# Kernel tuning notes

Measured on AMD Instinct MI355X. Metric: run time of the kernel, lower is better.

Reference implementation:

```python
import jax, jax.numpy as jnp
import numpy as np

K_MASK = -2.3819763e+38
B, T, D = 1, 2048, 3584
N, KH, H = 28, 4, 128  # query heads, kv heads, head_dim
ROPE_THETA = 1000000.0


def _rope_tables(t, h, theta):
    pos = jnp.arange(t, dtype=jnp.float32)[:, None]
    freq = theta ** (-jnp.arange(0, h, 2, dtype=jnp.float32) / h)[None, :]
    ang = pos * freq  # (T, H/2)
    return jnp.sin(ang)[None], jnp.cos(ang)[None]  # (1, T, H/2)


def apply_rotary_embedding(x, sin, cos):
    # x: (B,T,heads,H); sin/cos: (B,T,H/2)
    x1, x2 = x[..., : x.shape[-1] // 2], x[..., x.shape[-1] // 2 :]
    s, c = sin[:, :, None, :], cos[:, :, None, :]
    return jnp.concatenate([x1 * c - x2 * s, x2 * c + x1 * s], axis=-1)


def setup_inputs() -> dict:
    key = jax.random.key(0)
    ks = jax.random.split(key, 8)
    x = jax.random.normal(ks[0], (B, T, D), jnp.float32)
    attn_mask = jnp.tril(jnp.ones((T, T), jnp.bool_))[None]  # causal (B,T,S)
    sin, cos = _rope_tables(T, H, ROPE_THETA)
    std = 0.02
    wq = jax.random.normal(ks[1], (D, N, H), jnp.float32) * std
    wk = jax.random.normal(ks[2], (D, KH, H), jnp.float32) * std
    wv = jax.random.normal(ks[3], (D, KH, H), jnp.float32) * std
    wo = jax.random.normal(ks[4], (N, H, D), jnp.float32) * std
    q_bias = jax.random.normal(ks[5], (N * H,), jnp.float32) * std
    k_bias = jax.random.normal(ks[6], (KH * H,), jnp.float32) * std
    v_bias = jax.random.normal(ks[7], (KH * H,), jnp.float32) * std
    return {"x": x, "attn_mask": attn_mask, "sin": sin, "cos": cos,
            "wq": wq, "wk": wk, "wv": wv, "wo": wo,
            "q_bias": q_bias, "k_bias": k_bias, "v_bias": v_bias}


def reference(x, attn_mask, sin, cos, wq, wk, wv, wo, q_bias, k_bias, v_bias):
    b, t, _ = x.shape
    q = jnp.einsum('BTD,DNH->BTNH', x, wq) + q_bias.reshape(1, 1, N, H)
    k = jnp.einsum('BSD,DKH->BSKH', x, wk) + k_bias.reshape(1, 1, KH, H)
    v = jnp.einsum('BSD,DKH->BSKH', x, wv) + v_bias.reshape(1, 1, KH, H)
    q = apply_rotary_embedding(q, sin, cos)
    k = apply_rotary_embedding(k, sin, cos)
    g = N // KH  # GQA group size
    scale = H ** -0.5
    qg = q.reshape(b, t, KH, g, H)
    attn = jnp.einsum('BTHGD,BSHD->BHGTS', qg, k) * scale  # no KV repetition
    attn = attn.reshape(b, N, t, t)
    attn = jnp.where(attn_mask[:, None, :, :], attn, K_MASK)
    attn = jax.nn.softmax(attn.astype(jnp.float32), axis=-1).astype(k.dtype)
    attn = attn.reshape(b, KH, g, t, t)
    qkv = jnp.einsum('BHGTS,BSHD->BTHGD', attn, v).reshape(b, t, N, H)
    return jnp.einsum('BTNH,NHD->BTD', qkv, wo)
```

## Files before the change

kernel.cpp:

```cpp
#include <hip/hip_runtime.h>
#include <hip/hip_bf16.h>
#include <math.h>

#define Tn 2048
#define Dn 3584
#define NH 28
#define KHn 4
#define Hn 128
#define Gn 7
#define SCALE 0.08838834764831845f
#define LDC 4608
#define KOFF 3584
#define VOFF 4096
#define FBQ 128
#define FBS 64
#define NSPLIT 2
#define EXP_SHIFT 12.0f

typedef unsigned short u16;
typedef __attribute__((ext_vector_type(8))) short short8;
typedef __attribute__((ext_vector_type(4))) float floatx4;

__device__ __forceinline__ float bf_lo(unsigned int u) {
    union { unsigned int i; float f; } x; x.i = u << 16; return x.f;
}
__device__ __forceinline__ u16 f2bf(float f) {
    __hip_bfloat16 h = __float2bfloat16(f);
    return *reinterpret_cast<u16*>(&h);
}

__global__ void cast_f32_bf16(const float* __restrict__ in, u16* __restrict__ out, int n4)
{
    const int idx = blockIdx.x * blockDim.x + threadIdx.x;
    if (idx >= n4) return;
    const float4 f = ((const float4*)in)[idx];
    ((ushort4*)out)[idx] = make_ushort4(f2bf(f.x), f2bf(f.y), f2bf(f.z), f2bf(f.w));
}

__global__ __launch_bounds__(256) void transpose_cast(
    const float* __restrict__ in, u16* __restrict__ out, int R, int C, int ldo)
{
    __shared__ float ts[32][33];
    const int tid = threadIdx.x;
    const int c0 = blockIdx.x * 32, r0 = blockIdx.y * 32;
    const int tx = tid & 31, ty = tid >> 5;
    #pragma unroll
    for (int i = 0; i < 4; ++i)
        ts[ty + i * 8][tx] = in[(size_t)(r0 + ty + i * 8) * C + c0 + tx];
    __syncthreads();
    #pragma unroll
    for (int i = 0; i < 4; ++i)
        out[(size_t)(c0 + ty + i * 8) * ldo + r0 + tx] = f2bf(ts[tx][ty + i * 8]);
}

__global__ __launch_bounds__(256) void transpose_v(
    const u16* __restrict__ qkv, u16* __restrict__ vt)
{
    __shared__ u16 ts[32][33];
    const int tid = threadIdx.x;
    const int s0 = blockIdx.x * 32, d0 = blockIdx.y * 32;
    const int tx = tid & 31, ty = tid >> 5;
    #pragma unroll
    for (int i = 0; i < 4; ++i)
        ts[ty + i * 8][tx] = qkv[(size_t)(s0 + ty + i * 8) * LDC + VOFF + d0 + tx];
    __syncthreads();
    #pragma unroll
    for (int i = 0; i < 4; ++i)
        vt[(size_t)(d0 + ty + i * 8) * Tn + s0 + tx] = ts[tx][ty + i * 8];
}

__global__ void concat_bias(const float* __restrict__ qb, const float* __restrict__ kb,
                            const float* __restrict__ vb, float* __restrict__ out)
{
    const int j = blockIdx.x * blockDim.x + threadIdx.x;
    if (j >= 4608) return;
    out[j] = j < 3584 ? qb[j] : (j < 4096 ? kb[j - 3584] : vb[j - 4096]);
}

#define GM 128
#define GN 128
#define GK 32

__device__ __forceinline__ void async16(const void* g, void* l) {
    __builtin_amdgcn_global_load_lds(
        (const __attribute__((address_space(1))) unsigned int*)g,
        (__attribute__((address_space(3))) unsigned int*)l, 16, 0, 0);
}

template <typename OUT_T>
__global__ __launch_bounds__(256) void gemm_bf16_mfma(
    const u16* __restrict__ A, const u16* __restrict__ Bt,
    const float* __restrict__ bias, OUT_T* __restrict__ C,
    int M, int N, int K, int ldc)
{
    __shared__ __align__(16) u16 As[GM * GK];
    __shared__ __align__(16) u16 Bs[GN * GK];

    const int tid  = threadIdx.x;
    const int lane = tid & 63;
    const int wave = tid >> 6;
    const int wr = wave >> 1, wc = wave & 1;
    const int m16 = lane & 15, quad = lane >> 4;

    const int bm = blockIdx.y * GM;
    const int bn = blockIdx.x * GN;

    floatx4 acc[4][4];
    #pragma unroll
    for (int i = 0; i < 4; ++i)
        #pragma unroll
        for (int j = 0; j < 4; ++j) acc[i][j] = (floatx4)0.f;

    const int rl   = lane >> 2;
    const int kcol = (lane & 3) * 8;

    for (int k0 = 0; k0 < K; k0 += GK) {
        __syncthreads();
        #pragma unroll
        for (int i = 0; i < 2; ++i) {
            const int c = wave + i * 4;
            const int row = c * 16 + rl;
            async16(A  + (size_t)(bm + row) * K + k0 + kcol, &As[c * 512]);
            async16(Bt + (size_t)(bn + row) * K + k0 + kcol, &Bs[c * 512]);
        }
        __builtin_amdgcn_s_waitcnt(0);
        __syncthreads();

        short8 af[4], bfr[4];
        #pragma unroll
        for (int i = 0; i < 4; ++i)
            af[i] = *(const short8*)&As[(wr * 64 + i * 16 + m16) * GK + quad * 8];
        #pragma unroll
        for (int j = 0; j < 4; ++j)
            bfr[j] = *(const short8*)&Bs[(wc * 64 + j * 16 + m16) * GK + quad * 8];
        #pragma unroll
        for (int i = 0; i < 4; ++i)
            #pragma unroll
            for (int j = 0; j < 4; ++j)
                acc[i][j] = __builtin_amdgcn_mfma_f32_16x16x32_bf16(
                    af[i], bfr[j], acc[i][j], 0, 0, 0);
    }

    #pragma unroll
    for (int j = 0; j < 4; ++j) {
        const int col = bn + wc * 64 + j * 16 + m16;
        const float bv = bias ? bias[col] : 0.f;
        #pragma unroll
        for (int i = 0; i < 4; ++i) {
            const int rbase = bm + wr * 64 + i * 16 + quad * 4;
            #pragma unroll
            for (int r = 0; r < 4; ++r) {
                const float v = acc[i][j][r] + bv;
                if constexpr (sizeof(OUT_T) == 2)
                    C[(size_t)(rbase + r) * ldc + col] = (OUT_T)f2bf(v);
                else
                    C[(size_t)(rbase + r) * ldc + col] = v;
            }
        }
    }
}

__global__ void rope_bf16(u16* __restrict__ base,
                          const float* __restrict__ sin_t,
                          const float* __restrict__ cos_t,
                          int heads)
{
    const int idx = blockIdx.x * blockDim.x + threadIdx.x;
    const int n_elem = Tn * heads * 64;
    if (idx >= n_elem) return;
    const int i = idx & 63;
    const int h = (idx >> 6) % heads;
    const int t = idx / (64 * heads);
    const float s = sin_t[t * 64 + i];
    const float c = cos_t[t * 64 + i];
    u16* p = base + (size_t)t * LDC + h * Hn;
    const float x1 = bf_lo((unsigned int)p[i]);
    const float x2 = bf_lo((unsigned int)p[i + 64]);
    p[i]      = f2bf(x1 * c - x2 * s);
    p[i + 64] = f2bf(x2 * c + x1 * s);
}

__global__ __launch_bounds__(256, 2) void flash_attn_mfma(
    const u16* __restrict__ qkv, const u16* __restrict__ vt,
    float* __restrict__ po0, float* __restrict__ po1,
    float* __restrict__ lb)
{
    const int qt = (int)(gridDim.x - 1 - blockIdx.x);
    const int n  = blockIdx.y;
    const int z  = blockIdx.z;
    const int kh = n / Gn;
    const int tid  = threadIdx.x;
    const int lane = tid & 63;
    const int w    = tid >> 6;
    const int m16  = lane & 15;
    const int quad = lane >> 4;

    __shared__ __align__(16) u16 smem[64 * 136 + 128 * 72 + 128 * 72];
    u16* Ks = smem;
    u16* Vs = smem + 64 * 136;
    u16* Ps = Vs + 128 * 72;

    short8 qf[2][4];
    #pragma unroll
    for (int p = 0; p < 2; ++p) {
        const int qrow = qt * FBQ + w * 32 + p * 16 + m16;
        const u16* qp = qkv + (size_t)qrow * LDC + n * Hn;
        #pragma unroll
        for (int kc = 0; kc < 4; ++kc)
            qf[p][kc] = *(const short8*)(qp + kc * 32 + quad * 8);
    }

    floatx4 oacc[2][8];
    #pragma unroll
    for (int p = 0; p < 2; ++p)
        #pragma unroll
        for (int jn = 0; jn < 8; ++jn) oacc[p][jn] = (floatx4)0.f;
    float lrow[2][4];
    #pragma unroll
    for (int p = 0; p < 2; ++p)
        #pragma unroll
        for (int r = 0; r < 4; ++r) lrow[p][r] = 0.f;

    const int krow = tid >> 2, kseg = tid & 3;
    const int vrow = tid >> 1, vseg = tid & 1;
    const int st0 = z * (qt + 1);
    const int st1 = st0 + qt + 1;

    uint4 kv[4], vv[4];
    {
        const u16* kp = qkv + (size_t)(st0 * FBS + krow) * LDC + KOFF + kh * Hn + kseg * 32;
        #pragma unroll
        for (int i = 0; i < 4; ++i) kv[i] = *(const uint4*)(kp + i * 8);
        const u16* vp = vt + (size_t)(kh * Hn + vrow) * Tn + st0 * FBS + vseg * 32;
        #pragma unroll
        for (int i = 0; i < 4; ++i) vv[i] = *(const uint4*)(vp + i * 8);
    }

    for (int st = st0; st < st1; ++st) {
        __syncthreads();
        #pragma unroll
        for (int i = 0; i < 4; ++i)
            *(uint4*)&Ks[krow * 136 + kseg * 32 + i * 8] = kv[i];
        #pragma unroll
        for (int i = 0; i < 4; ++i)
            *(uint4*)&Vs[vrow * 72 + vseg * 32 + i * 8] = vv[i];
        __syncthreads();

        {
            const int pst = (st + 1 < st1) ? st + 1 : st1 - 1;
            const u16* kp = qkv + (size_t)(pst * FBS + krow) * LDC + KOFF + kh * Hn + kseg * 32;
            #pragma unroll
            for (int i = 0; i < 4; ++i) kv[i] = *(const uint4*)(kp + i * 8);
            const u16* vp = vt + (size_t)(kh * Hn + vrow) * Tn + pst * FBS + vseg * 32;
            #pragma unroll
            for (int i = 0; i < 4; ++i) vv[i] = *(const uint4*)(vp + i * 8);
        }

        const bool active = (st * FBS) <= (qt * FBQ + w * 32 + 31);
        if (active) {
            floatx4 sacc[2][4];
            #pragma unroll
            for (int p = 0; p < 2; ++p)
                #pragma unroll
                for (int j = 0; j < 4; ++j) sacc[p][j] = (floatx4)0.f;
            #pragma unroll
            for (int j = 0; j < 4; ++j) {
                #pragma unroll
                for (int kc = 0; kc < 4; ++kc) {
                    const short8 bfv = *(const short8*)&Ks[(j * 16 + m16) * 136 + kc * 32 + quad * 8];
                    sacc[0][j] = __builtin_amdgcn_mfma_f32_16x16x32_bf16(qf[0][kc], bfv, sacc[0][j], 0, 0, 0);
                    sacc[1][j] = __builtin_amdgcn_mfma_f32_16x16x32_bf16(qf[1][kc], bfv, sacc[1][j], 0, 0, 0);
                }
            }

            const bool diag = (st >= 2 * qt);
            #pragma unroll
            for (int p = 0; p < 2; ++p) {
                #pragma unroll
                for (int r = 0; r < 4; ++r) {
                    const int prow = w * 32 + p * 16 + quad * 4 + r;
                    const int row  = qt * FBQ + prow;
                    float ls = 0.f;
                    #pragma unroll
                    for (int j = 0; j < 4; ++j) {
                        float s = sacc[p][j][r] * SCALE - EXP_SHIFT;
                        if (diag && (st * FBS + j * 16 + m16 > row)) s = -1.0e30f;
                        const float e = __expf(s);
                        ls += e;
                        Ps[prow * 72 + j * 16 + m16] = f2bf(e);
                    }
                    lrow[p][r] += ls;
                }
            }

            #pragma unroll
            for (int kc2 = 0; kc2 < 2; ++kc2) {
                const short8 af0 = *(const short8*)&Ps[(w * 32 + m16) * 72 + kc2 * 32 + quad * 8];
                const short8 af1 = *(const short8*)&Ps[(w * 32 + 16 + m16) * 72 + kc2 * 32 + quad * 8];
                #pragma unroll
                for (int jn = 0; jn < 8; ++jn) {
                    const short8 bfv = *(const short8*)&Vs[(jn * 16 + m16) * 72 + kc2 * 32 + quad * 8];
                    oacc[0][jn] = __builtin_amdgcn_mfma_f32_16x16x32_bf16(af0, bfv, oacc[0][jn], 0, 0, 0);
                    oacc[1][jn] = __builtin_amdgcn_mfma_f32_16x16x32_bf16(af1, bfv, oacc[1][jn], 0, 0, 0);
                }
            }
        }
    }

    float lsum[2][4];
    #pragma unroll
    for (int p = 0; p < 2; ++p)
        #pragma unroll
        for (int r = 0; r < 4; ++r) {
            float l = lrow[p][r];
            l += __shfl_xor(l, 1); l += __shfl_xor(l, 2);
            l += __shfl_xor(l, 4); l += __shfl_xor(l, 8);
            lsum[p][r] = l;
        }

    if (m16 == 0) {
        #pragma unroll
        for (int p = 0; p < 2; ++p)
            #pragma unroll
            for (int r = 0; r < 4; ++r) {
                const int row = qt * FBQ + w * 32 + p * 16 + quad * 4 + r;
                lb[((size_t)z * NH + n) * Tn + row] = lsum[p][r];
            }
    }

    float* po = z ? po1 : po0;
    #pragma unroll
    for (int p = 0; p < 2; ++p)
        #pragma unroll
        for (int r = 0; r < 4; ++r) {
            const int grow = qt * FBQ + w * 32 + p * 16 + quad * 4 + r;
            float* pr = po + (size_t)grow * Dn + n * Hn + m16;
            #pragma unroll
            for (int jn = 0; jn < 8; ++jn)
                pr[jn * 16] = oacc[p][jn][r];
        }
}

__global__ __launch_bounds__(256) void combine_splits(
    const float* __restrict__ po0, const float* __restrict__ po1,
    const float* __restrict__ lb, u16* __restrict__ ob)
{
    const int idx = blockIdx.x * blockDim.x + threadIdx.x;
    const int n4  = Tn * Dn / 4;
    if (idx >= n4) return;
    const int c4  = idx % (Dn / 4);
    const int row = idx / (Dn / 4);
    const int n   = (c4 * 4) / Hn;

    const float l0 = lb[(size_t)n * Tn + row];
    const float l1 = lb[(size_t)(NH + n) * Tn + row];
    const float dn_ = 1.0f / (l0 + l1);

    const float4 v0 = ((const float4*)po0)[idx];
    const float4 v1 = ((const float4*)po1)[idx];
    ushort4 o;
    o.x = f2bf((v0.x + v1.x) * dn_);
    o.y = f2bf((v0.y + v1.y) * dn_);
    o.z = f2bf((v0.z + v1.z) * dn_);
    o.w = f2bf((v0.w + v1.w) * dn_);
    ((ushort4*)ob)[idx] = o;
}

extern "C" void kernel_launch(void* const* d_in, const int* in_sizes, int n_in,
                              void* d_out, int out_size, void* d_ws, size_t ws_size,
                              hipStream_t stream)
{
    const float* x      = (const float*)d_in[0];
    const float* sin_t  = (const float*)d_in[2];
    const float* cos_t  = (const float*)d_in[3];
    const float* wq     = (const float*)d_in[4];
    const float* wk     = (const float*)d_in[5];
    const float* wv     = (const float*)d_in[6];
    const float* wo     = (const float*)d_in[7];
    const float* q_bias = (const float*)d_in[8];
    const float* k_bias = (const float*)d_in[9];
    const float* v_bias = (const float*)d_in[10];
    float* out = (float*)d_out;

    char* ws = (char*)d_ws;
    u16*  cqkv = (u16*)ws;
    u16*  abuf = (u16*)(ws + 18874368);
    u16*  wt   = (u16*)(ws + 18874368 + 14680064);
    float* bqkv = (float*)(ws + 66584576);
    u16*  vtg  = wt;
    float* po0 = (float*)d_out;
    float* po1 = (float*)(ws + 35651584);
    float* lbf = (float*)(ws + 65011712);
    u16*  xb   = (u16*)d_out;

    cast_f32_bf16<<<(Tn * Dn / 4 + 255) / 256, 256, 0, stream>>>(x, xb, Tn * Dn / 4);
    transpose_cast<<<dim3(Dn / 32, Dn / 32), 256, 0, stream>>>(wq, wt, Dn, Dn, Dn);
    transpose_cast<<<dim3(512 / 32, Dn / 32), 256, 0, stream>>>(wk, wt + (size_t)KOFF * Dn, Dn, 512, Dn);
    transpose_cast<<<dim3(512 / 32, Dn / 32), 256, 0, stream>>>(wv, wt + (size_t)VOFF * Dn, Dn, 512, Dn);
    concat_bias<<<18, 256, 0, stream>>>(q_bias, k_bias, v_bias, bqkv);

    gemm_bf16_mfma<u16><<<dim3(LDC / GN, Tn / GM), 256, 0, stream>>>(
        xb, wt, bqkv, cqkv, Tn, LDC, Dn, LDC);

    rope_bf16<<<(Tn * 32 * 64 + 255) / 256, 256, 0, stream>>>(cqkv, sin_t, cos_t, 32);

    transpose_v<<<dim3(Tn / 32, 512 / 32), 256, 0, stream>>>(cqkv, vtg);

    flash_attn_mfma<<<dim3(Tn / FBQ, NH, NSPLIT), 256, 0, stream>>>(
        cqkv, vtg, po0, po1, lbf);

    combine_splits<<<(Tn * Dn / 4 + 255) / 256, 256, 0, stream>>>(po0, po1, lbf, abuf);

    transpose_cast<<<dim3(Dn / 32, Dn / 32), 256, 0, stream>>>(wo, wt, Dn, Dn, Dn);
    gemm_bf16_mfma<float><<<dim3(Dn / GN, Tn / GM), 256, 0, stream>>>(
        abuf, wt, nullptr, out, Tn, Dn, Dn, Dn);
}
```

Measured before the change: 605.4 us.

## Balance causal flash attention with table-driven variable KV splits and bf16 partials

Replaces the fixed two-way KV split with a lookup table that gives each query tile one to four chunks of at most eight KV tiles. This evens out per-block work under the causal mask and spreads it over more workgroups. Partial outputs are normalized and stored as bf16 rather than fp32, which halves partial-output traffic, and the combine step weights them by their row sums. The GEMM also gains an XCD-aware block-index swizzle to improve cache locality, at the cost of an extra zeroing kernel and some added bf16 rounding.

```diff
diff --git a/kernel.cpp b/kernel.cpp
--- a/kernel.cpp
+++ b/kernel.cpp
@@ -14,12 +14,21 @@
 #define VOFF 4096
 #define FBQ 128
 #define FBS 64
-#define NSPLIT 2
+#define MAXT 8
 #define EXP_SHIFT 12.0f
 
 typedef unsigned short u16;
 typedef __attribute__((ext_vector_type(8))) short short8;
 typedef __attribute__((ext_vector_type(4))) float floatx4;
+
+__device__ __constant__ unsigned char QT_TAB[40] = {
+    15,15,15,15, 14,14,14, 13,13,13, 12,12,12, 11,11,11,
+    10,10, 9,9, 8,8, 7,7, 6, 5, 4, 3,
+    14,10,6,2, 13,9,5,1, 12,8,4,0};
+__device__ __constant__ unsigned char S_TAB[40] = {
+     0, 1, 2, 3,  0, 1, 2,  0, 1, 2,  0, 1, 2,  0, 1, 2,
+     0, 1, 0,1, 0,1, 0,1, 0, 0, 0, 0,
+     3, 2,1,0,  3,2,1,0,  3,2,1,0};
 
 __device__ __forceinline__ float bf_lo(unsigned int u) {
     union { unsigned int i; float f; } x; x.i = u << 16; return x.f;
@@ -35,6 +44,12 @@
     if (idx >= n4) return;
     const float4 f = ((const float4*)in)[idx];
     ((ushort4*)out)[idx] = make_ushort4(f2bf(f.x), f2bf(f.y), f2bf(f.z), f2bf(f.w));
+}
+
+__global__ void zero_f32(float* __restrict__ p, int n)
+{
+    const int i = blockIdx.x * blockDim.x + threadIdx.x;
+    if (i < n) p[i] = 0.f;
 }
 
 __global__ __launch_bounds__(256) void transpose_cast(
@@ -102,8 +117,12 @@
     const int wr = wave >> 1, wc = wave & 1;
     const int m16 = lane & 15, quad = lane >> 4;
 
-    const int bm = blockIdx.y * GM;
-    const int bn = blockIdx.x * GN;
+    const int nwg = gridDim.x * gridDim.y;
+    const int bid = blockIdx.y * gridDim.x + blockIdx.x;
+    const int cpx = nwg >> 3;
+    const int swz = (bid & 7) * cpx + (bid >> 3);
+    const int bm = (swz / gridDim.x) * GM;
+    const int bn = (swz % gridDim.x) * GN;
 
     floatx4 acc[4][4];
     #pragma unroll
@@ -182,12 +201,12 @@
 
 __global__ __launch_bounds__(256, 2) void flash_attn_mfma(
     const u16* __restrict__ qkv, const u16* __restrict__ vt,
-    float* __restrict__ po0, float* __restrict__ po1,
+    u16* __restrict__ pb01, u16* __restrict__ pb23,
     float* __restrict__ lb)
 {
-    const int qt = (int)(gridDim.x - 1 - blockIdx.x);
+    const int qt = (int)QT_TAB[blockIdx.x];
+    const int s  = (int)S_TAB[blockIdx.x];
     const int n  = blockIdx.y;
-    const int z  = blockIdx.z;
     const int kh = n / Gn;
     const int tid  = threadIdx.x;
     const int lane = tid & 63;
@@ -223,8 +242,9 @@
 
     const int krow = tid >> 2, kseg = tid & 3;
     const int vrow = tid >> 1, vseg = tid & 1;
-    const int st0 = z * (qt + 1);
-    const int st1 = st0 + qt + 1;
+    const int nst = 2 * qt + 2;
+    const int st0 = s * MAXT;
+    const int st1 = (st0 + MAXT < nst) ? st0 + MAXT : nst;
 
     uint4 kv[4], vv[4];
     {
@@ -283,9 +303,9 @@
                     float ls = 0.f;
                     #pragma unroll
                     for (int j = 0; j < 4; ++j) {
-                        float s = sacc[p][j][r] * SCALE - EXP_SHIFT;
-                        if (diag && (st * FBS + j * 16 + m16 > row)) s = -1.0e30f;
-                        const float e = __expf(s);
+                        float sv = sacc[p][j][r] * SCALE - EXP_SHIFT;
+                        if (diag && (st * FBS + j * 16 + m16 > row)) sv = -1.0e30f;
+                        const float e = __expf(sv);
                         ls += e;
                         Ps[prow * 72 + j * 16 + m16] = f2bf(e);
                     }
@@ -307,7 +327,7 @@
         }
     }
 
-    float lsum[2][4];
+    float lsum[2][4], invl[2][4];
     #pragma unroll
     for (int p = 0; p < 2; ++p)
         #pragma unroll
@@ -316,6 +336,7 @@
             l += __shfl_xor(l, 1); l += __shfl_xor(l, 2);
             l += __shfl_xor(l, 4); l += __shfl_xor(l, 8);
             lsum[p][r] = l;
+            invl[p][r] = (l > 0.f) ? 1.0f / l : 0.f;
         }
 
     if (m16 == 0) {
@@ -324,25 +345,26 @@
             #pragma unroll
             for (int r = 0; r < 4; ++r) {
                 const int row = qt * FBQ + w * 32 + p * 16 + quad * 4 + r;
-                lb[((size_t)z * NH + n) * Tn + row] = lsum[p][r];
+                lb[((size_t)s * NH + n) * Tn + row] = lsum[p][r];
             }
     }
 
-    float* po = z ? po1 : po0;
+    u16* po = (s < 2) ? pb01 + (size_t)s * Tn * Dn
+                      : pb23 + (size_t)(s - 2) * Tn * Dn;
     #pragma unroll
     for (int p = 0; p < 2; ++p)
         #pragma unroll
         for (int r = 0; r < 4; ++r) {
             const int grow = qt * FBQ + w * 32 + p * 16 + quad * 4 + r;
-            float* pr = po + (size_t)grow * Dn + n * Hn + m16;
+            u16* pr = po + (size_t)grow * Dn + n * Hn + m16;
             #pragma unroll
             for (int jn = 0; jn < 8; ++jn)
-                pr[jn * 16] = oacc[p][jn][r];
+                pr[jn * 16] = f2bf(oacc[p][jn][r] * invl[p][r]);
         }
 }
 
 __global__ __launch_bounds__(256) void combine_splits(
-    const float* __restrict__ po0, const float* __restrict__ po1,
+    const u16* __restrict__ pb01, const u16* __restrict__ pb23,
     const float* __restrict__ lb, u16* __restrict__ ob)
 {
     const int idx = blockIdx.x * blockDim.x + threadIdx.x;
@@ -350,19 +372,29 @@
     if (idx >= n4) return;
     const int c4  = idx % (Dn / 4);
     const int row = idx / (Dn / 4);
-    const int n   = (c4 * 4) / Hn;
-
-    const float l0 = lb[(size_t)n * Tn + row];
-    const float l1 = lb[(size_t)(NH + n) * Tn + row];
-    const float dn_ = 1.0f / (l0 + l1);
-
-    const float4 v0 = ((const float4*)po0)[idx];
-    const float4 v1 = ((const float4*)po1)[idx];
+    const int n   = (c4 * 4) >> 7;
+
+    float den = 0.f, ax = 0.f, ay = 0.f, az = 0.f, aw = 0.f;
+    #pragma unroll
+    for (int s = 0; s < 4; ++s) {
+        const float l = lb[((size_t)s * NH + n) * Tn + row];
+        if (l > 0.f) {
+            const u16* p = (s < 2) ? pb01 + (size_t)s * Tn * Dn
+                                   : pb23 + (size_t)(s - 2) * Tn * Dn;
+            const ushort4 v = ((const ushort4*)p)[idx];
+            den += l;
+            ax += l * bf_lo((unsigned int)v.x);
+            ay += l * bf_lo((unsigned int)v.y);
+            az += l * bf_lo((unsigned int)v.z);
+            aw += l * bf_lo((unsigned int)v.w);
+        }
+    }
+    const float inv = 1.0f / den;
     ushort4 o;
-    o.x = f2bf((v0.x + v1.x) * dn_);
-    o.y = f2bf((v0.y + v1.y) * dn_);
-    o.z = f2bf((v0.z + v1.z) * dn_);
-    o.w = f2bf((v0.w + v1.w) * dn_);
+    o.x = f2bf(ax * inv);
+    o.y = f2bf(ay * inv);
+    o.z = f2bf(az * inv);
+    o.w = f2bf(aw * inv);
     ((ushort4*)ob)[idx] = o;
 }
 
@@ -388,8 +420,8 @@
     u16*  wt   = (u16*)(ws + 18874368 + 14680064);
     float* bqkv = (float*)(ws + 66584576);
     u16*  vtg  = wt;
-    float* po0 = (float*)d_out;
-    float* po1 = (float*)(ws + 35651584);
+    u16*  pb01 = (u16*)d_out;
+    u16*  pb23 = (u16*)(ws + 35651584);
     float* lbf = (float*)(ws + 65011712);
     u16*  xb   = (u16*)d_out;
 
@@ -402,14 +434,16 @@
     gemm_bf16_mfma<u16><<<dim3(LDC / GN, Tn / GM), 256, 0, stream>>>(
         xb, wt, bqkv, cqkv, Tn, LDC, Dn, LDC);
 
+    zero_f32<<<(4 * NH * Tn + 255) / 256, 256, 0, stream>>>(lbf, 4 * NH * Tn);
+
     rope_bf16<<<(Tn * 32 * 64 + 255) / 256, 256, 0, stream>>>(cqkv, sin_t, cos_t, 32);
 
     transpose_v<<<dim3(Tn / 32, 512 / 32), 256, 0, stream>>>(cqkv, vtg);
 
-    flash_attn_mfma<<<dim3(Tn / FBQ, NH, NSPLIT), 256, 0, stream>>>(
-        cqkv, vtg, po0, po1, lbf);
-
-    combine_splits<<<(Tn * Dn / 4 + 255) / 256, 256, 0, stream>>>(po0, po1, lbf, abuf);
+    flash_attn_mfma<<<dim3(40, NH), 256, 0, stream>>>(
+        cqkv, vtg, pb01, pb23, lbf);
+
+    combine_splits<<<(Tn * Dn / 4 + 255) / 256, 256, 0, stream>>>(pb01, pb23, lbf, abuf);
 
     transpose_cast<<<dim3(Dn / 32, Dn / 32), 256, 0, stream>>>(wo, wt, Dn, Dn, Dn);
     gemm_bf16_mfma<float><<<dim3(Dn / GN, Tn / GM), 256, 0, stream>>>(
```

Result: faster. 562.2 us (-7.1%).
